# Optimization experiments

Measured on AMD Instinct MI355X. Metric: run time of the kernel, lower is better.

## Reference

```python
import jax, jax.numpy as jnp
import numpy as np


def setup_inputs() -> dict:
    key = jax.random.key(0)
    ks = jax.random.split(key, 5)
    B, S, D, H, dk = 4, 2048, 1024, 16, 64
    s = 0.02
    return {
        "x": jax.random.normal(ks[0], (B, S, D), dtype=jnp.float32),
        "Wq": jax.random.normal(ks[1], (H, D, dk), dtype=jnp.float32) * s,
        "Wk": jax.random.normal(ks[2], (H, D, dk), dtype=jnp.float32) * s,
        "Wv": jax.random.normal(ks[3], (H, D, dk), dtype=jnp.float32) * s,
        "Wo": jax.random.normal(ks[4], (H * dk, D), dtype=jnp.float32) * s,
    }


def reference(x, Wq, Wk, Wv, Wo):
    # Per-head projections: [B,S,D] x [H,D,dk] -> [B,H,S,dk]
    Q = jnp.einsum("bsd,hdk->bhsk", x, Wq)
    K = jnp.einsum("bsd,hdk->bhsk", x, Wk)
    V = jnp.einsum("bsd,hdk->bhsk", x, Wv)
    scale = 1.0 / jnp.sqrt(jnp.asarray(Wq.shape[-1], x.dtype))
    scores = jnp.einsum("bhqk,bhsk->bhqs", Q, K) * scale  # [B,H,S,S]
    attn = jax.nn.softmax(scores, axis=-1)
    out = jnp.einsum("bhqs,bhsk->bhqk", attn, V)  # [B,H,S,dk]
    B, H, S, dk = out.shape
    # concat heads along feature dim (matches torch.cat over head outputs)
    out = out.transpose(0, 2, 1, 3).reshape(B, S, H * dk)
    return out @ Wo  # [B,S,D]
```

## Files before the change

### kernel.cpp

```cpp
#include <hip/hip_runtime.h>
#include <hip/hip_bf16.h>
#include <stdint.h>

typedef __attribute__((ext_vector_type(8))) short bf16x8;
typedef __attribute__((ext_vector_type(4))) float f32x4;
typedef __attribute__((ext_vector_type(4))) unsigned short us4;

#define AS1C(p) ((const __attribute__((address_space(1))) void*)(p))
#define AS3(p)  ((__attribute__((address_space(3))) void*)(p))

#if __has_builtin(__builtin_amdgcn_exp2f)
#define EXP2(x) __builtin_amdgcn_exp2f(x)
#else
#define EXP2(x) __expf((x) * 0.69314718f)
#endif

#define MAX3(a,b,c) fmaxf(fmaxf((a),(b)),(c))

static __device__ __forceinline__ unsigned short f2b(float f) {
  union { __hip_bfloat16 h; unsigned short u; } cv;
  cv.h = __float2bfloat16(f);
  return cv.u;
}

static __device__ __forceinline__ unsigned int cvtpk(float a, float b) {
  unsigned int r;
  asm("v_cvt_pk_bf16_f32 %0, %1, %2" : "=v"(r) : "v"(a), "v"(b));
  return r;
}

__global__ __launch_bounds__(256) void conv_x_kernel(const float* __restrict__ x,
                                                     unsigned short* __restrict__ xb,
                                                     int n4) {
  int i = blockIdx.x * 256 + threadIdx.x;
  if (i >= n4) return;
  float4 v = ((const float4*)x)[i];
  us4 r = { f2b(v.x), f2b(v.y), f2b(v.z), f2b(v.w) };
  *(us4*)&xb[(size_t)i * 4] = r;
}

__global__ __launch_bounds__(256) void conv_wqkv_kernel(const float* __restrict__ Wq,
                                                        const float* __restrict__ Wk,
                                                        const float* __restrict__ Wv,
                                                        unsigned short* __restrict__ WqkvT) {
  int bid = blockIdx.x;
  int which = bid >> 8;
  int h  = (bid >> 4) & 15;
  int dt = bid & 15;
  const float* W = (which == 0) ? Wq : (which == 1 ? Wk : Wv);
  __shared__ float tile[64][65];
  const int t = threadIdx.x;
  const int c  = t & 63;
  const int r0 = t >> 6;
  const float* src = W + (size_t)h * 65536 + (size_t)dt * 64 * 64;
#pragma unroll
  for (int it = 0; it < 16; ++it) {
    int r = r0 + it * 4;
    tile[r][c] = src[r * 64 + c];
  }
  __syncthreads();
  const size_t n0 = (size_t)which * 1024 + h * 64;
  const int d0 = dt * 64;
#pragma unroll
  for (int it = 0; it < 16; ++it) {
    int cc = r0 + it * 4;
    WqkvT[(n0 + cc) * 1024 + d0 + c] = f2b(tile[c][cc]);
  }
}

__global__ __launch_bounds__(256) void conv_wo_kernel(const float* __restrict__ Wo,
                                                      unsigned short* __restrict__ WoT) {
  int kt = blockIdx.x >> 4, nt = blockIdx.x & 15;
  __shared__ float tile[64][65];
  const int t = threadIdx.x;
  const int c  = t & 63;
  const int r0 = t >> 6;
  const float* src = Wo + (size_t)(kt * 64) * 1024 + nt * 64;
#pragma unroll
  for (int it = 0; it < 16; ++it) {
    int r = r0 + it * 4;
    tile[r][c] = src[(size_t)r * 1024 + c];
  }
  __syncthreads();
#pragma unroll
  for (int it = 0; it < 16; ++it) {
    int cc = r0 + it * 4;
    WoT[((size_t)nt * 64 + cc) * 1024 + kt * 64 + c] = f2b(tile[c][cc]);
  }
}

__global__ __launch_bounds__(256) void gemm_qkv_kernel(
    const unsigned short* __restrict__ A,
    const unsigned short* __restrict__ Bt,
    unsigned short* __restrict__ Q,
    unsigned short* __restrict__ Ko,
    unsigned short* __restrict__ Vt) {
  __shared__ __align__(16) unsigned short sA[128 * 32];
  __shared__ __align__(16) unsigned short sB[128 * 32];
  const int tid  = threadIdx.x;
  const int lane = tid & 63;
  const int wid  = tid >> 6;
  const int wr = wid >> 1, wc = wid & 1;
  const int brow = blockIdx.y * 128;
  const int bcol = blockIdx.x * 128;
  const int K = 1024;

  f32x4 acc[4][4] = {};

  const int r4 = tid >> 2;
  const int c8 = (tid & 3) * 8;
  const unsigned short* ga = A  + (size_t)(brow + r4) * K + c8;
  const unsigned short* gb = Bt + (size_t)(bcol + r4) * K + c8;
  unsigned short* lAw = sA + wid * 512;
  unsigned short* lBw = sB + wid * 512;

  for (int kb = 0; kb < K; kb += 32) {
    if (kb) __syncthreads();
    __builtin_amdgcn_global_load_lds(AS1C(ga + kb),            AS3(lAw),        16, 0, 0);
    __builtin_amdgcn_global_load_lds(AS1C(ga + 64 * K + kb),   AS3(lAw + 2048), 16, 0, 0);
    __builtin_amdgcn_global_load_lds(AS1C(gb + kb),            AS3(lBw),        16, 0, 0);
    __builtin_amdgcn_global_load_lds(AS1C(gb + 64 * K + kb),   AS3(lBw + 2048), 16, 0, 0);
    __syncthreads();

    bf16x8 af[4], bfr[4];
#pragma unroll
    for (int mi = 0; mi < 4; ++mi)
      af[mi] = *(const bf16x8*)&sA[(wr * 64 + mi * 16 + (lane & 15)) * 32 + (lane >> 4) * 8];
#pragma unroll
    for (int ni = 0; ni < 4; ++ni)
      bfr[ni] = *(const bf16x8*)&sB[(wc * 64 + ni * 16 + (lane & 15)) * 32 + (lane >> 4) * 8];
#pragma unroll
    for (int mi = 0; mi < 4; ++mi)
#pragma unroll
      for (int ni = 0; ni < 4; ++ni)
        acc[mi][ni] = __builtin_amdgcn_mfma_f32_16x16x32_bf16(af[mi], bfr[ni], acc[mi][ni], 0, 0, 0);
  }

#pragma unroll
  for (int mi = 0; mi < 4; ++mi) {
    int row0 = brow + wr * 64 + mi * 16 + (lane >> 4) * 4;
    int b = row0 >> 11, s0 = row0 & 2047;
#pragma unroll
    for (int ni = 0; ni < 4; ++ni) {
      int col = bcol + wc * 64 + ni * 16 + (lane & 15);
      int which = col >> 10;
      int h  = (col >> 6) & 15;
      int kk = col & 63;
      if (which == 2) {
        us4 pk = { f2b(acc[mi][ni][0]), f2b(acc[mi][ni][1]),
                   f2b(acc[mi][ni][2]), f2b(acc[mi][ni][3]) };
        *(us4*)&Vt[((size_t)(b * 16 + h) * 64 + kk) * 2048 + s0] = pk;
      } else {
        unsigned short* dst = (which == 0) ? Q : Ko;
        float scl = (which == 0) ? 0.18033688f : 1.0f;
#pragma unroll
        for (int j = 0; j < 4; ++j)
          dst[((size_t)(b * 16 + h) * 2048 + (s0 + j)) * 64 + kk] = f2b(acc[mi][ni][j] * scl);
      }
    }
  }
}

__global__ __launch_bounds__(256) void gemm_out_kernel(
    const unsigned short* __restrict__ A,
    const unsigned short* __restrict__ Bt,
    float* __restrict__ out) {
  __shared__ __align__(16) unsigned short sA[128 * 32];
  __shared__ __align__(16) unsigned short sB[128 * 32];
  const int tid  = threadIdx.x;
  const int lane = tid & 63;
  const int wid  = tid >> 6;
  const int wr = wid >> 1, wc = wid & 1;
  const int brow = blockIdx.y * 128;
  const int bcol = blockIdx.x * 128;
  const int K = 1024;

  f32x4 acc[4][4] = {};

  const int r4 = tid >> 2;
  const int c8 = (tid & 3) * 8;
  const unsigned short* ga = A  + (size_t)(brow + r4) * K + c8;
  const unsigned short* gb = Bt + (size_t)(bcol + r4) * K + c8;
  unsigned short* lAw = sA + wid * 512;
  unsigned short* lBw = sB + wid * 512;

  for (int kb = 0; kb < K; kb += 32) {
    if (kb) __syncthreads();
    __builtin_amdgcn_global_load_lds(AS1C(ga + kb),          AS3(lAw),        16, 0, 0);
    __builtin_amdgcn_global_load_lds(AS1C(ga + 64 * K + kb), AS3(lAw + 2048), 16, 0, 0);
    __builtin_amdgcn_global_load_lds(AS1C(gb + kb),          AS3(lBw),        16, 0, 0);
    __builtin_amdgcn_global_load_lds(AS1C(gb + 64 * K + kb), AS3(lBw + 2048), 16, 0, 0);
    __syncthreads();

    bf16x8 af[4], bfr[4];
#pragma unroll
    for (int mi = 0; mi < 4; ++mi)
      af[mi] = *(const bf16x8*)&sA[(wr * 64 + mi * 16 + (lane & 15)) * 32 + (lane >> 4) * 8];
#pragma unroll
    for (int ni = 0; ni < 4; ++ni)
      bfr[ni] = *(const bf16x8*)&sB[(wc * 64 + ni * 16 + (lane & 15)) * 32 + (lane >> 4) * 8];
#pragma unroll
    for (int mi = 0; mi < 4; ++mi)
#pragma unroll
      for (int ni = 0; ni < 4; ++ni)
        acc[mi][ni] = __builtin_amdgcn_mfma_f32_16x16x32_bf16(af[mi], bfr[ni], acc[mi][ni], 0, 0, 0);
  }

#pragma unroll
  for (int mi = 0; mi < 4; ++mi) {
    int row0 = brow + wr * 64 + mi * 16 + (lane >> 4) * 4;
#pragma unroll
    for (int ni = 0; ni < 4; ++ni) {
      int col = bcol + wc * 64 + ni * 16 + (lane & 15);
#pragma unroll
      for (int j = 0; j < 4; ++j)
        out[(size_t)(row0 + j) * 1024 + col] = acc[mi][ni][j];
    }
  }
}

__global__ __launch_bounds__(512) void attn_kernel(
    const unsigned short* __restrict__ Q,
    const unsigned short* __restrict__ K,
    const unsigned short* __restrict__ Vt,
    unsigned short* __restrict__ O) {
  __shared__ __align__(16) unsigned short sK[2][64 * 64];
  __shared__ __align__(16) unsigned short sVt[2][64 * 64];
  __shared__ __align__(16) unsigned short sP[8][16 * 72];

  const int tid = threadIdx.x, lane = tid & 63, w = tid >> 6;
  const int l15 = lane & 15, hi = lane >> 4;
  const int n = blockIdx.x + (blockIdx.y << 4);
  const int bh = (n & 7) * 8 + ((n >> 3) >> 4);
  const int qx = (n >> 3) & 15;
  const int qb = qx * 128;
  const unsigned short* Qp  = Q  + (size_t)bh * 131072;
  const unsigned short* Kp  = K  + (size_t)bh * 131072;
  const unsigned short* Vtp = Vt + (size_t)bh * 131072;

  const int qrow = qb + w * 16 + l15;
  bf16x8 qf0 = *(const bf16x8*)&Qp[(size_t)qrow * 64 + hi * 8];
  bf16x8 qf1 = *(const bf16x8*)&Qp[(size_t)qrow * 64 + 32 + hi * 8];

  f32x4 o[4] = {};
  float m_ = 0.f;
  float l_ = 0.f;

  const int lrow = lane >> 3;
  const int uch  = (lane & 7) ^ lrow;
  const unsigned short* kg = Kp  + (size_t)(w * 8 + lrow) * 64   + uch * 8;
  const unsigned short* vg = Vtp + (size_t)(w * 8 + lrow) * 2048 + uch * 8;
  unsigned short* dK0 = &sK[0][w * 512];
  unsigned short* dK1 = &sK[1][w * 512];
  unsigned short* dV0 = &sVt[0][w * 512];
  unsigned short* dV1 = &sVt[1][w * 512];

  const int x7 = l15 & 7;
  const int ck0 = (hi ^ x7) * 8;
  const int ck1 = ((hi + 4) ^ x7) * 8;

  __builtin_amdgcn_global_load_lds(AS1C(kg), AS3(dK0), 16, 0, 0);
  __builtin_amdgcn_global_load_lds(AS1C(vg), AS3(dV0), 16, 0, 0);
  __syncthreads();

  for (int kt = 0; kt < 32; ++kt) {
    const int cur = kt & 1;
    if (kt < 31) {
      kg += 4096; vg += 64;
      __builtin_amdgcn_global_load_lds(AS1C(kg), AS3(cur ? dK0 : dK1), 16, 0, 0);
      __builtin_amdgcn_global_load_lds(AS1C(vg), AS3(cur ? dV0 : dV1), 16, 0, 0);
    }
    const unsigned short* sKc  = &sK[cur][0];
    const unsigned short* sVtc = &sVt[cur][0];

    f32x4 sc[4] = {};
    __builtin_amdgcn_s_setprio(1);
#pragma unroll
    for (int ni = 0; ni < 4; ++ni) {
      bf16x8 kf0 = *(const bf16x8*)&sKc[(ni * 16 + l15) * 64 + ck0];
      bf16x8 kf1 = *(const bf16x8*)&sKc[(ni * 16 + l15) * 64 + ck1];
      sc[ni] = __builtin_amdgcn_mfma_f32_16x16x32_bf16(kf0, qf0, sc[ni], 0, 0, 0);
      sc[ni] = __builtin_amdgcn_mfma_f32_16x16x32_bf16(kf1, qf1, sc[ni], 0, 0, 0);
    }
    __builtin_amdgcn_s_setprio(0);

    float t0 = MAX3(sc[0][0], sc[0][1], sc[0][2]);
    float t1 = MAX3(sc[0][3], sc[1][0], sc[1][1]);
    float t2 = MAX3(sc[1][2], sc[1][3], sc[2][0]);
    float t3 = MAX3(sc[2][1], sc[2][2], sc[2][3]);
    float t4 = MAX3(sc[3][0], sc[3][1], sc[3][2]);
    float pmax = fmaxf(MAX3(t0, t1, t2), MAX3(t3, t4, sc[3][3]));

    if (!__all(pmax - m_ <= 8.0f)) {
      pmax = fmaxf(pmax, __shfl_xor(pmax, 16));
      pmax = fmaxf(pmax, __shfl_xor(pmax, 32));
      float mnew  = fmaxf(m_, pmax);
      float alpha = EXP2(m_ - mnew);
      l_ *= alpha;
#pragma unroll
      for (int j = 0; j < 4; ++j) {
        float aj = __shfl(alpha, hi * 4 + j);
#pragma unroll
        for (int ni = 0; ni < 4; ++ni) o[ni][j] *= aj;
      }
      m_ = mnew;
    }

    const float mcur = m_;
    f32x4 sum4 = {};
#pragma unroll
    for (int ni = 0; ni < 4; ++ni)
#pragma unroll
      for (int r = 0; r < 4; ++r) {
        float p = EXP2(sc[ni][r] - mcur);
        sc[ni][r] = p;
        sum4[r] += p;
      }
    l_ += (sum4[0] + sum4[1]) + (sum4[2] + sum4[3]);

    unsigned short* pb = &sP[w][l15 * 72];
#pragma unroll
    for (int ni = 0; ni < 4; ++ni) {
      uint2 pk = { cvtpk(sc[ni][0], sc[ni][1]), cvtpk(sc[ni][2], sc[ni][3]) };
      *(uint2*)&pb[ni * 16 + hi * 4] = pk;
    }

    bf16x8 pa0 = *(const bf16x8*)&sP[w][l15 * 72 + hi * 8];
    bf16x8 pa1 = *(const bf16x8*)&sP[w][l15 * 72 + 32 + hi * 8];
    __builtin_amdgcn_s_setprio(1);
#pragma unroll
    for (int ni = 0; ni < 4; ++ni) {
      bf16x8 vf0 = *(const bf16x8*)&sVtc[(ni * 16 + l15) * 64 + ck0];
      bf16x8 vf1 = *(const bf16x8*)&sVtc[(ni * 16 + l15) * 64 + ck1];
      o[ni] = __builtin_amdgcn_mfma_f32_16x16x32_bf16(pa0, vf0, o[ni], 0, 0, 0);
      o[ni] = __builtin_amdgcn_mfma_f32_16x16x32_bf16(pa1, vf1, o[ni], 0, 0, 0);
    }
    __builtin_amdgcn_s_setprio(0);

    __syncthreads();
  }

  l_ += __shfl_xor(l_, 16);
  l_ += __shfl_xor(l_, 32);
  float linv = 1.0f / l_;

  const int b = bh >> 4, h = bh & 15;
#pragma unroll
  for (int j = 0; j < 4; ++j) {
    float inv = __shfl(linv, hi * 4 + j);
    int row = qb + w * 16 + hi * 4 + j;
#pragma unroll
    for (int ni = 0; ni < 4; ++ni)
      O[((size_t)b * 2048 + row) * 1024 + h * 64 + ni * 16 + l15] = f2b(o[ni][j] * inv);
  }
}

extern "C" void kernel_launch(void* const* d_in, const int* in_sizes, int n_in,
                              void* d_out, int out_size, void* d_ws, size_t ws_size,
                              hipStream_t stream) {
  const float* x  = (const float*)d_in[0];
  const float* Wq = (const float*)d_in[1];
  const float* Wk = (const float*)d_in[2];
  const float* Wv = (const float*)d_in[3];
  const float* Wo = (const float*)d_in[4];
  float* out = (float*)d_out;

  char* w = (char*)d_ws;
  unsigned short* xb   = (unsigned short*)(w);
  unsigned short* wqkv = (unsigned short*)(w + 16777216);
  unsigned short* wo   = (unsigned short*)(w + 23068672);
  unsigned short* Qb   = (unsigned short*)(w + 25165824);
  unsigned short* Kb   = (unsigned short*)(w + 41943040);
  unsigned short* Vtb  = (unsigned short*)(w + 58720256);
  unsigned short* Ob   = (unsigned short*)(w + 75497472);

  conv_x_kernel<<<8192, 256, 0, stream>>>(x, xb, 2097152);
  conv_wqkv_kernel<<<768, 256, 0, stream>>>(Wq, Wk, Wv, wqkv);
  conv_wo_kernel<<<256, 256, 0, stream>>>(Wo, wo);
  gemm_qkv_kernel<<<dim3(24, 64), 256, 0, stream>>>(xb, wqkv, Qb, Kb, Vtb);
  attn_kernel<<<dim3(16, 64), 512, 0, stream>>>(Qb, Kb, Vtb, Ob);
  gemm_out_kernel<<<dim3(8, 64), 256, 0, stream>>>(Ob, wo, out);
}
```

Measured before the change: 199.7 us.

## Process two query tiles per wave in attention and swizzle GEMM block order

The attention kernel now has each wave handle 32 query rows (two 16-row tiles) instead of 16, so each block covers 256 queries and every K/V tile loaded into LDS is reused across twice as many queries. The grid is halved to match. Both GEMM kernels also remap block indices so consecutive blocks are spread across XCD-style groups, aiming for better L2 locality. The cost is more registers per wave for accumulators, which may lower occupancy, and fewer attention blocks in flight.

```diff
diff --git a/kernel.cpp b/kernel.cpp
--- a/kernel.cpp
+++ b/kernel.cpp
@@ -101,8 +101,10 @@
   const int lane = tid & 63;
   const int wid  = tid >> 6;
   const int wr = wid >> 1, wc = wid & 1;
-  const int brow = blockIdx.y * 128;
-  const int bcol = blockIdx.x * 128;
+  const int n0 = blockIdx.y * 24 + blockIdx.x;
+  const int n1 = (n0 & 7) * 192 + (n0 >> 3);
+  const int brow = (n1 / 24) * 128;
+  const int bcol = (n1 % 24) * 128;
   const int K = 1024;
 
   f32x4 acc[4][4] = {};
@@ -171,8 +173,10 @@
   const int lane = tid & 63;
   const int wid  = tid >> 6;
   const int wr = wid >> 1, wc = wid & 1;
-  const int brow = blockIdx.y * 128;
-  const int bcol = blockIdx.x * 128;
+  const int n0 = blockIdx.y * 8 + blockIdx.x;
+  const int n1 = (n0 & 7) * 64 + (n0 >> 3);
+  const int brow = (n1 >> 3) * 128;
+  const int bcol = (n1 & 7) * 128;
   const int K = 1024;
 
   f32x4 acc[4][4] = {};
@@ -226,25 +230,29 @@
     unsigned short* __restrict__ O) {
   __shared__ __align__(16) unsigned short sK[2][64 * 64];
   __shared__ __align__(16) unsigned short sVt[2][64 * 64];
-  __shared__ __align__(16) unsigned short sP[8][16 * 72];
+  __shared__ __align__(16) unsigned short sP[16][16 * 72];
 
   const int tid = threadIdx.x, lane = tid & 63, w = tid >> 6;
   const int l15 = lane & 15, hi = lane >> 4;
-  const int n = blockIdx.x + (blockIdx.y << 4);
-  const int bh = (n & 7) * 8 + ((n >> 3) >> 4);
-  const int qx = (n >> 3) & 15;
-  const int qb = qx * 128;
+  const int n = blockIdx.x + (blockIdx.y << 3);
+  const int bh = (n & 7) * 8 + (n >> 6);
+  const int qx = (n >> 3) & 7;
+  const int qb = qx * 256;
   const unsigned short* Qp  = Q  + (size_t)bh * 131072;
   const unsigned short* Kp  = K  + (size_t)bh * 131072;
   const unsigned short* Vtp = Vt + (size_t)bh * 131072;
 
-  const int qrow = qb + w * 16 + l15;
-  bf16x8 qf0 = *(const bf16x8*)&Qp[(size_t)qrow * 64 + hi * 8];
-  bf16x8 qf1 = *(const bf16x8*)&Qp[(size_t)qrow * 64 + 32 + hi * 8];
-
-  f32x4 o[4] = {};
-  float m_ = 0.f;
-  float l_ = 0.f;
+  bf16x8 qf[2][2];
+#pragma unroll
+  for (int mi = 0; mi < 2; ++mi) {
+    int qrow = qb + w * 32 + mi * 16 + l15;
+    qf[mi][0] = *(const bf16x8*)&Qp[(size_t)qrow * 64 + hi * 8];
+    qf[mi][1] = *(const bf16x8*)&Qp[(size_t)qrow * 64 + 32 + hi * 8];
+  }
+
+  f32x4 o[2][4] = {};
+  float m_[2] = { 0.f, 0.f };
+  float l_[2] = { 0.f, 0.f };
 
   const int lrow = lane >> 3;
   const int uch  = (lane & 7) ^ lrow;
@@ -273,85 +281,98 @@
     const unsigned short* sKc  = &sK[cur][0];
     const unsigned short* sVtc = &sVt[cur][0];
 
-    f32x4 sc[4] = {};
-    __builtin_amdgcn_s_setprio(1);
-#pragma unroll
-    for (int ni = 0; ni < 4; ++ni) {
-      bf16x8 kf0 = *(const bf16x8*)&sKc[(ni * 16 + l15) * 64 + ck0];
-      bf16x8 kf1 = *(const bf16x8*)&sKc[(ni * 16 + l15) * 64 + ck1];
-      sc[ni] = __builtin_amdgcn_mfma_f32_16x16x32_bf16(kf0, qf0, sc[ni], 0, 0, 0);
-      sc[ni] = __builtin_amdgcn_mfma_f32_16x16x32_bf16(kf1, qf1, sc[ni], 0, 0, 0);
-    }
-    __builtin_amdgcn_s_setprio(0);
-
-    float t0 = MAX3(sc[0][0], sc[0][1], sc[0][2]);
-    float t1 = MAX3(sc[0][3], sc[1][0], sc[1][1]);
-    float t2 = MAX3(sc[1][2], sc[1][3], sc[2][0]);
-    float t3 = MAX3(sc[2][1], sc[2][2], sc[2][3]);
-    float t4 = MAX3(sc[3][0], sc[3][1], sc[3][2]);
-    float pmax = fmaxf(MAX3(t0, t1, t2), MAX3(t3, t4, sc[3][3]));
-
-    if (!__all(pmax - m_ <= 8.0f)) {
-      pmax = fmaxf(pmax, __shfl_xor(pmax, 16));
-      pmax = fmaxf(pmax, __shfl_xor(pmax, 32));
-      float mnew  = fmaxf(m_, pmax);
-      float alpha = EXP2(m_ - mnew);
-      l_ *= alpha;
-#pragma unroll
-      for (int j = 0; j < 4; ++j) {
-        float aj = __shfl(alpha, hi * 4 + j);
-#pragma unroll
-        for (int ni = 0; ni < 4; ++ni) o[ni][j] *= aj;
+#pragma unroll
+    for (int mi = 0; mi < 2; ++mi) {
+      f32x4 sc[4] = {};
+      __builtin_amdgcn_s_setprio(1);
+#pragma unroll
+      for (int ni = 0; ni < 4; ++ni) {
+        bf16x8 kf0 = *(const bf16x8*)&sKc[(ni * 16 + l15) * 64 + ck0];
+        bf16x8 kf1 = *(const bf16x8*)&sKc[(ni * 16 + l15) * 64 + ck1];
+        sc[ni] = __builtin_amdgcn_mfma_f32_16x16x32_bf16(kf0, qf[mi][0], sc[ni], 0, 0, 0);
+        sc[ni] = __builtin_amdgcn_mfma_f32_16x16x32_bf16(kf1, qf[mi][1], sc[ni], 0, 0, 0);
       }
-      m_ = mnew;
-    }
-
-    const float mcur = m_;
-    f32x4 sum4 = {};
-#pragma unroll
-    for (int ni = 0; ni < 4; ++ni)
-#pragma unroll
-      for (int r = 0; r < 4; ++r) {
-        float p = EXP2(sc[ni][r] - mcur);
-        sc[ni][r] = p;
-        sum4[r] += p;
+      __builtin_amdgcn_s_setprio(0);
+
+      float t0 = MAX3(sc[0][0], sc[0][1], sc[0][2]);
+      float t1 = MAX3(sc[0][3], sc[1][0], sc[1][1]);
+      float t2 = MAX3(sc[1][2], sc[1][3], sc[2][0]);
+      float t3 = MAX3(sc[2][1], sc[2][2], sc[2][3]);
+      float t4 = MAX3(sc[3][0], sc[3][1], sc[3][2]);
+      float pmax = fmaxf(MAX3(t0, t1, t2), MAX3(t3, t4, sc[3][3]));
+
+      if (!__all(pmax - m_[mi] <= 8.0f)) {
+        pmax = fmaxf(pmax, __shfl_xor(pmax, 16));
+        pmax = fmaxf(pmax, __shfl_xor(pmax, 32));
+        float mnew  = fmaxf(m_[mi], pmax);
+        float alpha = EXP2(m_[mi] - mnew);
+        l_[mi] *= alpha;
+#pragma unroll
+        for (int j = 0; j < 4; ++j) {
+          float aj = __shfl(alpha, hi * 4 + j);
+#pragma unroll
+          for (int ni = 0; ni < 4; ++ni) o[mi][ni][j] *= aj;
+        }
+        m_[mi] = mnew;
       }
-    l_ += (sum4[0] + sum4[1]) + (sum4[2] + sum4[3]);
-
-    unsigned short* pb = &sP[w][l15 * 72];
-#pragma unroll
-    for (int ni = 0; ni < 4; ++ni) {
-      uint2 pk = { cvtpk(sc[ni][0], sc[ni][1]), cvtpk(sc[ni][2], sc[ni][3]) };
-      *(uint2*)&pb[ni * 16 + hi * 4] = pk;
-    }
-
-    bf16x8 pa0 = *(const bf16x8*)&sP[w][l15 * 72 + hi * 8];
-    bf16x8 pa1 = *(const bf16x8*)&sP[w][l15 * 72 + 32 + hi * 8];
+
+      const float mcur = m_[mi];
+      f32x4 sum4 = {};
+#pragma unroll
+      for (int ni = 0; ni < 4; ++ni)
+#pragma unroll
+        for (int r = 0; r < 4; ++r) {
+          float p = EXP2(sc[ni][r] - mcur);
+          sc[ni][r] = p;
+          sum4[r] += p;
+        }
+      l_[mi] += (sum4[0] + sum4[1]) + (sum4[2] + sum4[3]);
+
+      unsigned short* pb = &sP[w * 2 + mi][l15 * 72];
+#pragma unroll
+      for (int ni = 0; ni < 4; ++ni) {
+        uint2 pk = { cvtpk(sc[ni][0], sc[ni][1]), cvtpk(sc[ni][2], sc[ni][3]) };
+        *(uint2*)&pb[ni * 16 + hi * 4] = pk;
+      }
+    }
+
+    bf16x8 pa[2][2];
+#pragma unroll
+    for (int mi = 0; mi < 2; ++mi) {
+      pa[mi][0] = *(const bf16x8*)&sP[w * 2 + mi][l15 * 72 + hi * 8];
+      pa[mi][1] = *(const bf16x8*)&sP[w * 2 + mi][l15 * 72 + 32 + hi * 8];
+    }
     __builtin_amdgcn_s_setprio(1);
 #pragma unroll
     for (int ni = 0; ni < 4; ++ni) {
       bf16x8 vf0 = *(const bf16x8*)&sVtc[(ni * 16 + l15) * 64 + ck0];
       bf16x8 vf1 = *(const bf16x8*)&sVtc[(ni * 16 + l15) * 64 + ck1];
-      o[ni] = __builtin_amdgcn_mfma_f32_16x16x32_bf16(pa0, vf0, o[ni], 0, 0, 0);
-      o[ni] = __builtin_amdgcn_mfma_f32_16x16x32_bf16(pa1, vf1, o[ni], 0, 0, 0);
+#pragma unroll
+      for (int mi = 0; mi < 2; ++mi) {
+        o[mi][ni] = __builtin_amdgcn_mfma_f32_16x16x32_bf16(pa[mi][0], vf0, o[mi][ni], 0, 0, 0);
+        o[mi][ni] = __builtin_amdgcn_mfma_f32_16x16x32_bf16(pa[mi][1], vf1, o[mi][ni], 0, 0, 0);
+      }
     }
     __builtin_amdgcn_s_setprio(0);
 
     __syncthreads();
   }
 
-  l_ += __shfl_xor(l_, 16);
-  l_ += __shfl_xor(l_, 32);
-  float linv = 1.0f / l_;
-
   const int b = bh >> 4, h = bh & 15;
 #pragma unroll
-  for (int j = 0; j < 4; ++j) {
-    float inv = __shfl(linv, hi * 4 + j);
-    int row = qb + w * 16 + hi * 4 + j;
-#pragma unroll
-    for (int ni = 0; ni < 4; ++ni)
-      O[((size_t)b * 2048 + row) * 1024 + h * 64 + ni * 16 + l15] = f2b(o[ni][j] * inv);
+  for (int mi = 0; mi < 2; ++mi) {
+    float lm = l_[mi];
+    lm += __shfl_xor(lm, 16);
+    lm += __shfl_xor(lm, 32);
+    float linv = 1.0f / lm;
+#pragma unroll
+    for (int j = 0; j < 4; ++j) {
+      float inv = __shfl(linv, hi * 4 + j);
+      int row = qb + w * 32 + mi * 16 + hi * 4 + j;
+#pragma unroll
+      for (int ni = 0; ni < 4; ++ni)
+        O[((size_t)b * 2048 + row) * 1024 + h * 64 + ni * 16 + l15] = f2b(o[mi][ni][j] * inv);
+    }
   }
 }
 
@@ -378,6 +399,6 @@
   conv_wqkv_kernel<<<768, 256, 0, stream>>>(Wq, Wk, Wv, wqkv);
   conv_wo_kernel<<<256, 256, 0, stream>>>(Wo, wo);
   gemm_qkv_kernel<<<dim3(24, 64), 256, 0, stream>>>(xb, wqkv, Qb, Kb, Vtb);
-  attn_kernel<<<dim3(16, 64), 512, 0, stream>>>(Qb, Kb, Vtb, Ob);
+  attn_kernel<<<dim3(8, 64), 512, 0, stream>>>(Qb, Kb, Vtb, Ob);
   gemm_out_kernel<<<dim3(8, 64), 256, 0, stream>>>(Ob, wo, out);
 }
```

Measured after the change: 190.7 us. 4.5% less time.
